# Kernel optimization log

Hardware: AMD Instinct MI355X
Metric: run time of the kernel (lower is better)

The kernel has to match this reference:

```python
import jax, jax.numpy as jnp
import numpy as np

N_NODES = 50000
N_EDGES = 800000
NF = 64       # input_nf = output_nf = hidden_nf
RADIAL = 1

def tanhshrink(x):
    return x - jnp.tanh(x)

def _linear_params(key, fan_in, fan_out):
    k1, k2 = jax.random.split(key)
    s = 1.0 / np.sqrt(fan_in)
    W = jax.random.uniform(k1, (fan_in, fan_out), jnp.float32, -s, s)
    b = jax.random.uniform(k2, (fan_out,), jnp.float32, -s, s)
    return W, b

def setup_inputs() -> dict:
    key = jax.random.key(0)
    ks = jax.random.split(key, 11)
    nodes = jax.random.normal(ks[0], (N_NODES, NF), jnp.float32)
    coord = jax.random.normal(ks[1], (N_NODES, 3), jnp.float32)
    edges = jax.random.randint(ks[2], (2, N_EDGES), 0, N_NODES, jnp.int64)
    # Edge MLP: Linear(2*NF + RADIAL -> NF), Linear(NF -> NF)
    eW1, eb1 = _linear_params(ks[3], 2 * NF + RADIAL, NF)
    eW2, eb2 = _linear_params(ks[4], NF, NF)
    # Edge attention: Linear(2*NF -> NF), Linear(NF -> 1)
    aW1, ab1 = _linear_params(ks[5], 2 * NF, NF)
    aW2, ab2 = _linear_params(ks[6], NF, 1)
    # Node MLP: Linear(NF + NF -> NF), Linear(NF -> NF)
    nW1, nb1 = _linear_params(ks[7], 2 * NF, NF)
    nW2, nb2 = _linear_params(ks[8], NF, NF)
    # Coord MLP: Linear(NF -> NF), Linear(NF -> 1)
    cW1, cb1 = _linear_params(ks[9], NF, NF)
    cW2, cb2 = _linear_params(ks[10], NF, 1)
    return dict(nodes=nodes, coord=coord, edges=edges,
                eW1=eW1, eb1=eb1, eW2=eW2, eb2=eb2,
                aW1=aW1, ab1=ab1, aW2=aW2, ab2=ab2,
                nW1=nW1, nb1=nb1, nW2=nW2, nb2=nb2,
                cW1=cW1, cb1=cb1, cW2=cW2, cb2=cb2)

def reference(nodes, coord, edges,
              eW1, eb1, eW2, eb2,
              aW1, ab1, aW2, ab2,
              nW1, nb1, nW2, nb2,
              cW1, cb1, cW2, cb2):
    row, col = edges[0], edges[1]
    n = nodes.shape[0]
    # Radial: squared distance along each edge
    rij = coord[row] - coord[col]                       # [E, 3]
    radial = jnp.sum(rij * rij, axis=1, keepdims=True)  # [E, 1]
    src, tgt = nodes[row], nodes[col]                   # [E, NF]
    # Edge MLP with attention gate
    agg_in = jnp.concatenate([src, tgt, radial], axis=1)
    h = tanhshrink(agg_in @ eW1 + eb1)
    h = tanhshrink(h @ eW2 + eb2)                       # [E, NF]
    att_in = jnp.concatenate([src, tgt], axis=1)
    a = tanhshrink(att_in @ aW1 + ab1)
    a = jax.nn.sigmoid(a @ aW2 + ab2)                   # [E, 1]
    edge_feat = h * a                                   # [E, NF]
    # Coordinate update: rij scaled by scalar per edge, scatter-add to row
    c = tanhshrink(edge_feat @ cW1 + cb1)
    trans = rij * (c @ cW2 + cb2)                       # [E, 3]
    coord_out = coord + jax.ops.segment_sum(trans, row, num_segments=n)
    # Node update: scatter-add edge features to row, residual MLP
    agg = jax.ops.segment_sum(edge_feat, row, num_segments=n)  # [N, NF]
    m = jnp.concatenate([nodes, agg], axis=1)
    m = tanhshrink(m @ nW1 + nb1)
    nodes_out = nodes + (m @ nW2 + nb2)
    return nodes_out, coord_out
```

## Files before the change

### kernel.cpp

```cpp
#include <hip/hip_runtime.h>
#include <hip/hip_fp16.h>

#define NF 64

typedef _Float16 half8 __attribute__((ext_vector_type(8)));
typedef float f32x4 __attribute__((ext_vector_type(4)));

__device__ __forceinline__ float ts_f(float x){
  float t = __expf(2.0f*x);
  float th = 1.0f - 2.0f*__builtin_amdgcn_rcpf(t + 1.0f);
  return x - th;
}
__device__ __forceinline__ float sigmoid_f(float x){
  return __builtin_amdgcn_rcpf(1.0f + __expf(-x));
}

__global__ __launch_bounds__(256) void k_prepw_hist(
    const float* __restrict__ eW1, const float* __restrict__ aW1,
    const float* __restrict__ eW2, const float* __restrict__ cW1,
    const float* __restrict__ nW1, const float* __restrict__ nW2,
    _Float16* __restrict__ W256t, _Float16* __restrict__ N1t,
    _Float16* __restrict__ W2t, _Float16* __restrict__ C1t,
    _Float16* __restrict__ N2t,
    const int* __restrict__ edges, int* __restrict__ counts,
    int* __restrict__ rank, int E,
    float4* __restrict__ zagg, int naggf4,
    float4* __restrict__ zcoord, int ncoordf4,
    int histB)
{
  const int bi = blockIdx.x;
  if (bi < 64){
    const int t = bi*256 + threadIdx.x;
    {
      const int n = t >> 6, k = t & 63;
      float v;
      if      (n < 64)  v = eW1[k*NF + n];
      else if (n < 128) v = aW1[k*NF + (n-64)];
      else if (n < 192) v = eW1[(64+k)*NF + (n-128)];
      else              v = aW1[(64+k)*NF + (n-192)];
      W256t[t] = (_Float16)v;
    }
    if (t < 64*128){
      const int n = t >> 7, k = t & 127;
      N1t[t] = (_Float16)nW1[k*NF + n];
    }
    if (t < 64*64){
      const int n = t >> 6, k = t & 63;
      W2t[t] = (_Float16)eW2[k*NF + n];
      C1t[t] = (_Float16)cW1[k*NF + n];
      N2t[t] = (_Float16)nW2[k*NF + n];
    }
  } else if (bi < 64 + histB){
    const int e = (bi - 64)*256 + threadIdx.x;
    if (e < E) rank[e] = atomicAdd(&counts[edges[e]], 1);
  } else {
    const float4 z = make_float4(0.f,0.f,0.f,0.f);
    const int nthr = (gridDim.x - 64 - histB) * 256;
    const int tid = (bi - 64 - histB)*256 + threadIdx.x;
    for (int i = tid; i < naggf4; i += nthr)   zagg[i] = z;
    for (int i = tid; i < ncoordf4; i += nthr) zcoord[i] = z;
  }
}

__global__ __launch_bounds__(256) void k_scan_zero(
    const int* __restrict__ counts, int* __restrict__ offs,
    int* __restrict__ btot, int* __restrict__ btop, int* __restrict__ done,
    const int* __restrict__ sentinel,
    int SCAN_B)
{
  const int t = threadIdx.x;
  const int b = blockIdx.x;

  __shared__ int s[256];
  __shared__ int isLast;
  const int BASE = *sentinel;
  const int4 c = *(const int4*)(counts + b*1024 + 4*t);
  const int c0 = c.x - BASE, c1 = c.y - BASE, c2 = c.z - BASE, c3 = c.w - BASE;
  const int mysum = c0 + c1 + c2 + c3;
  s[t] = mysum; __syncthreads();
  #pragma unroll
  for (int d=1; d<256; d<<=1){
    const int v = (t>=d) ? s[t-d] : 0; __syncthreads();
    s[t] += v; __syncthreads();
  }
  const int base = (t==0) ? 0 : s[t-1];
  int4 o;
  o.x = base; o.y = base + c0; o.z = o.y + c1; o.w = o.z + c2;
  *(int4*)(offs + b*1024 + 4*t) = o;
  if (t == 255) btot[b] = s[255];

  __threadfence();
  if (t == 0) isLast = (atomicAdd(done, 1) == BASE + SCAN_B - 1);
  __syncthreads();
  if (isLast){
    __threadfence();
    const int v = (t < SCAN_B) ? btot[t] : 0;
    s[t] = v; __syncthreads();
    #pragma unroll
    for (int d=1; d<256; d<<=1){
      const int u = (t>=d) ? s[t-d] : 0; __syncthreads();
      s[t] += u; __syncthreads();
    }
    if (t < SCAN_B) btop[t] = (t==0) ? 0 : s[t-1];
  }
}

__global__ __launch_bounds__(64, 8) void k_pre_scatter(
    const float* __restrict__ nodes,
    const float* __restrict__ eb1, const float* __restrict__ ab1,
    const _Float16* __restrict__ W256t,
    _Float16* __restrict__ P, _Float16* __restrict__ Q, int N,
    const int* __restrict__ edges, const int* __restrict__ offs,
    const int* __restrict__ btop, const int* __restrict__ rank,
    const int* __restrict__ sentinel,
    int* __restrict__ rs, int* __restrict__ cs, int E,
    int preBlocks)
{
  const int bi = blockIdx.x;
  const int lane = threadIdx.x;
  if (bi >= preBlocks){
    const int BASE = *sentinel;
    const int e = (bi - preBlocks)*64 + lane;
    if (e < E){
      const int r = edges[e], c = edges[E + e];
      const int pos = btop[r >> 10] + offs[r] + (rank[e] - BASE);
      rs[pos] = r; cs[pos] = c;
    }
    return;
  }

  const int p = lane & 15, q = lane >> 4;
  const int m0 = bi * 16;
  const int row = m0 + p;

  const float* __restrict__ xr = nodes + (size_t)row * NF;
  half8 A[2];
  #pragma unroll
  for (int kt=0; kt<2; kt++){
    const float4 xa = *(const float4*)(xr + kt*32 + q*8);
    const float4 xb = *(const float4*)(xr + kt*32 + q*8 + 4);
    A[kt][0]=(_Float16)xa.x; A[kt][1]=(_Float16)xa.y; A[kt][2]=(_Float16)xa.z; A[kt][3]=(_Float16)xa.w;
    A[kt][4]=(_Float16)xb.x; A[kt][5]=(_Float16)xb.y; A[kt][6]=(_Float16)xb.z; A[kt][7]=(_Float16)xb.w;
  }

  #pragma unroll
  for (int ni=0; ni<16; ni++){
    float b = 0.f;
    if (ni < 4)       b = eb1[16*ni + p];
    else if (ni < 8)  b = ab1[16*(ni-4) + p];
    f32x4 acc = (f32x4){b,b,b,b};
    #pragma unroll
    for (int kt=0; kt<2; kt++){
      const half8 Bf = *(const half8*)(W256t + (size_t)(16*ni + p)*NF + kt*32 + q*8);
      acc = __builtin_amdgcn_mfma_f32_16x16x32_f16(A[kt], Bf, acc, 0,0,0);
    }
    _Float16* __restrict__ dst = (ni < 8 ? P : Q);
    const int colbase = (ni & 7) * 16 + p;
    #pragma unroll
    for (int rr=0; rr<4; rr++)
      dst[(size_t)(m0 + 4*q + rr)*128 + colbase] = (_Float16)acc[rr];
  }
}

__global__ __launch_bounds__(64, 4) void egcl_edge(
    const float* __restrict__ coord,
    const int*   __restrict__ rs, const int* __restrict__ cs,
    const _Float16* __restrict__ P, const _Float16* __restrict__ Q,
    const float* __restrict__ eW1,
    const _Float16* __restrict__ W2t, const float* __restrict__ eb2,
    const float* __restrict__ aW2, const float* __restrict__ ab2,
    const _Float16* __restrict__ C1t, const float* __restrict__ cb1,
    const float* __restrict__ cW2, const float* __restrict__ cb2,
    _Float16* __restrict__ aggh, float* __restrict__ coord_out,
    int E)
{
  __shared__ _Float16 tile[64][72];
  __shared__ float gcbuf[64];

  const int lane = threadIdx.x;
  const int p = lane & 15, q = lane >> 4;
  const int e = blockIdx.x * 64 + lane;
  const bool valid = (e < E);
  const int el = valid ? e : (E - 1);

  const int r = rs[el];
  const int c = cs[el];
  const int rv = valid ? r : -1;

  const float rx = coord[3*r+0] - coord[3*c+0];
  const float ry = coord[3*r+1] - coord[3*c+1];
  const float rz = coord[3*r+2] - coord[3*c+2];
  const float radial = rx*rx + ry*ry + rz*rz;

  const _Float16* __restrict__ Pr = P + (size_t)r * 128;
  const _Float16* __restrict__ Qc = Q + (size_t)c * 128;
  const float* __restrict__ wrad = eW1 + 128*NF;

  half8 Bf[4][2];
  #pragma unroll
  for (int ni=0;ni<4;ni++)
    #pragma unroll
    for (int kt=0;kt<2;kt++)
      Bf[ni][kt] = *(const half8*)(W2t + (size_t)(16*ni + p)*NF + kt*32 + q*8);

  float sp0=0.f, sp1=0.f;
  #pragma unroll
  for (int g=0;g<8;g++){
    const half8 pa = *(const half8*)(Pr + 64 + 8*g);
    const half8 qa = *(const half8*)(Qc + 64 + 8*g);
    #pragma unroll
    for (int j=0;j<8;j++){
      const float v = ts_f((float)pa[j] + (float)qa[j]);
      if (j & 1) sp1 = fmaf(v, aW2[8*g+j], sp1); else sp0 = fmaf(v, aW2[8*g+j], sp0);
    }
  }
  const float gate = sigmoid_f(sp0 + sp1 + ab2[0]);
  gcbuf[lane] = gate;

  #pragma unroll
  for (int g=0;g<8;g++){
    const half8 ph = *(const half8*)(Pr + 8*g);
    const half8 qh = *(const half8*)(Qc + 8*g);
    half8 hv;
    #pragma unroll
    for (int j=0;j<8;j++)
      hv[j] = (_Float16)ts_f(fmaf(radial, wrad[8*g+j], (float)ph[j] + (float)qh[j]));
    *(half8*)&tile[lane][8*g] = hv;
  }
  __syncthreads();

  f32x4 acc[4][4];
  #pragma unroll
  for (int ni=0;ni<4;ni++){
    const float b = eb2[16*ni + p];
    #pragma unroll
    for (int mi=0;mi<4;mi++) acc[mi][ni] = (f32x4){b,b,b,b};
  }
  #pragma unroll
  for (int mi=0;mi<4;mi++){
    #pragma unroll
    for (int kt=0;kt<2;kt++){
      const half8 Af = *(const half8*)&tile[16*mi + p][kt*32 + q*8];
      #pragma unroll
      for (int ni=0;ni<4;ni++)
        acc[mi][ni] = __builtin_amdgcn_mfma_f32_16x16x32_f16(Af, Bf[ni][kt], acc[mi][ni], 0,0,0);
    }
  }
  __syncthreads();

  #pragma unroll
  for (int mi=0;mi<4;mi++){
    #pragma unroll
    for (int rr=0;rr<4;rr++){
      const int row = 16*mi + 4*q + rr;
      const float gv = gcbuf[row];
      #pragma unroll
      for (int ni=0;ni<4;ni++)
        tile[row][16*ni + p] = (_Float16)(ts_f(acc[mi][ni][rr]) * gv);
    }
  }

  #pragma unroll
  for (int ni=0;ni<4;ni++)
    #pragma unroll
    for (int kt=0;kt<2;kt++)
      Bf[ni][kt] = *(const half8*)(C1t + (size_t)(16*ni + p)*NF + kt*32 + q*8);
  #pragma unroll
  for (int ni=0;ni<4;ni++){
    const float b = cb1[16*ni + p];
    #pragma unroll
    for (int mi=0;mi<4;mi++) acc[mi][ni] = (f32x4){b,b,b,b};
  }
  __syncthreads();
  #pragma unroll
  for (int mi=0;mi<4;mi++){
    #pragma unroll
    for (int kt=0;kt<2;kt++){
      const half8 Af = *(const half8*)&tile[16*mi + p][kt*32 + q*8];
      #pragma unroll
      for (int ni=0;ni<4;ni++)
        acc[mi][ni] = __builtin_amdgcn_mfma_f32_16x16x32_f16(Af, Bf[ni][kt], acc[mi][ni], 0,0,0);
    }
  }

  float part[4][4];
  {
    float w2c[4];
    #pragma unroll
    for (int ni=0;ni<4;ni++) w2c[ni] = cW2[16*ni + p];
    #pragma unroll
    for (int mi=0;mi<4;mi++)
      #pragma unroll
      for (int rr=0;rr<4;rr++){
        float s = 0.f;
        #pragma unroll
        for (int ni=0;ni<4;ni++) s = fmaf(ts_f(acc[mi][ni][rr]), w2c[ni], s);
        part[mi][rr] = s;
      }
  }
  #pragma unroll
  for (int mask=1; mask<16; mask<<=1)
    #pragma unroll
    for (int mi=0;mi<4;mi++)
      #pragma unroll
      for (int rr=0;rr<4;rr++)
        part[mi][rr] += __shfl_xor(part[mi][rr], mask);
  {
    float v = 0.f;
    #pragma unroll
    for (int mi=0;mi<4;mi++)
      #pragma unroll
      for (int rr=0;rr<4;rr++)
        if (((p>>2)==mi) & ((p&3)==rr)) v = part[mi][rr];
    gcbuf[16*(p>>2) + 4*q + (p&3)] = v + cb2[0];
  }
  __syncthreads();

  const float cse = gcbuf[lane];

  unsigned long long bmask;
  {
    const int rvp = __shfl_up(rv, 1);
    const int fl = (lane == 0) || (rv != rvp);
    bmask = __ballot(fl);
  }

  {
    float tx = rx * cse, ty = ry * cse, tz = rz * cse;
    const int s = 63 - __builtin_clzll(bmask & ((2ull << lane) - 1ull));
    #pragma unroll
    for (int d=1; d<64; d<<=1){
      const float ux = __shfl_up(tx, d);
      const float uy = __shfl_up(ty, d);
      const float uz = __shfl_up(tz, d);
      if (lane >= d && (lane - d) >= s){ tx += ux; ty += uy; tz += uz; }
    }
    const int tail = (lane == 63) || (((bmask >> ((lane + 1) & 63)) & 1ull) && lane < 63);
    if (tail && rv >= 0){
      atomicAdd(coord_out + 3*rv + 0, tx);
      atomicAdd(coord_out + 3*rv + 1, ty);
      atomicAdd(coord_out + 3*rv + 2, tz);
    }
  }

  {
    int cur_r = __shfl(rv, 0);
    float runsum = 0.f;
    #pragma unroll
    for (int g8=0; g8<8; ++g8){
      _Float16 v[8];
      #pragma unroll
      for (int i=0;i<8;i++) v[i] = tile[g8*8 + i][lane];
      #pragma unroll
      for (int i=0;i<8;i++){
        const int eo = g8*8 + i;
        if (eo > 0 && ((bmask >> eo) & 1ull)){
          const float v0 = __shfl(runsum, 2*lane);
          const float v1 = __shfl(runsum, 2*lane+1);
          if (cur_r >= 0 && lane < 32){
            __half2 hv; hv.x = __float2half(v0); hv.y = __float2half(v1);
            unsafeAtomicAdd((__half2*)aggh + (size_t)cur_r*32 + lane, hv);
          }
          runsum = 0.f;
          cur_r = __shfl(rv, eo);
        }
        runsum += (float)v[i];
      }
    }
    const float v0 = __shfl(runsum, 2*lane);
    const float v1 = __shfl(runsum, 2*lane+1);
    if (cur_r >= 0 && lane < 32){
      __half2 hv; hv.x = __float2half(v0); hv.y = __float2half(v1);
      unsafeAtomicAdd((__half2*)aggh + (size_t)cur_r*32 + lane, hv);
    }
  }
}

__global__ __launch_bounds__(64, 8) void egcl_node(
    const float* __restrict__ nodes, const float* __restrict__ coord,
    const _Float16* __restrict__ aggh,
    const _Float16* __restrict__ N1t, const float* __restrict__ nb1,
    const _Float16* __restrict__ N2t, const float* __restrict__ nb2,
    float* __restrict__ out_nodes, float* __restrict__ out_coord, int N)
{
  __shared__ _Float16 t2[16][72];
  const int lane = threadIdx.x;
  const int p = lane & 15, q = lane >> 4;
  const int m0 = blockIdx.x * 16;
  const int row = m0 + p;

  half8 A[4];
  const float* __restrict__ xr = nodes + (size_t)row * NF;
  #pragma unroll
  for (int kt=0; kt<2; kt++){
    const float4 xa = *(const float4*)(xr + kt*32 + q*8);
    const float4 xb = *(const float4*)(xr + kt*32 + q*8 + 4);
    A[kt][0]=(_Float16)xa.x; A[kt][1]=(_Float16)xa.y; A[kt][2]=(_Float16)xa.z; A[kt][3]=(_Float16)xa.w;
    A[kt][4]=(_Float16)xb.x; A[kt][5]=(_Float16)xb.y; A[kt][6]=(_Float16)xb.z; A[kt][7]=(_Float16)xb.w;
  }
  const _Float16* __restrict__ ar = aggh + (size_t)row * NF;
  #pragma unroll
  for (int kt=2; kt<4; kt++)
    A[kt] = *(const half8*)(ar + (kt-2)*32 + q*8);

  f32x4 acc[4];
  #pragma unroll
  for (int ni=0;ni<4;ni++){
    const float b = nb1[16*ni + p];
    acc[ni] = (f32x4){b,b,b,b};
  }
  #pragma unroll
  for (int kt=0; kt<4; kt++){
    #pragma unroll
    for (int ni=0;ni<4;ni++){
      const half8 Bf = *(const half8*)(N1t + (size_t)(16*ni + p)*128 + kt*32 + q*8);
      acc[ni] = __builtin_amdgcn_mfma_f32_16x16x32_f16(A[kt], Bf, acc[ni], 0,0,0);
    }
  }

  #pragma unroll
  for (int ni=0;ni<4;ni++)
    #pragma unroll
    for (int rr=0;rr<4;rr++)
      t2[4*q + rr][16*ni + p] = (_Float16)ts_f(acc[ni][rr]);
  __syncthreads();

  half8 A2[2];
  #pragma unroll
  for (int kt=0; kt<2; kt++)
    A2[kt] = *(const half8*)&t2[p][kt*32 + q*8];

  f32x4 acc2[4];
  #pragma unroll
  for (int ni=0;ni<4;ni++){
    const float b = nb2[16*ni + p];
    acc2[ni] = (f32x4){b,b,b,b};
  }
  #pragma unroll
  for (int kt=0; kt<2; kt++){
    #pragma unroll
    for (int ni=0;ni<4;ni++){
      const half8 Bf = *(const half8*)(N2t + (size_t)(16*ni + p)*NF + kt*32 + q*8);
      acc2[ni] = __builtin_amdgcn_mfma_f32_16x16x32_f16(A2[kt], Bf, acc2[ni], 0,0,0);
    }
  }

  #pragma unroll
  for (int ni=0;ni<4;ni++){
    #pragma unroll
    for (int rr=0;rr<4;rr++){
      const size_t idx = (size_t)(m0 + 4*q + rr)*NF + 16*ni + p;
      out_nodes[idx] = nodes[idx] + acc2[ni][rr];
    }
  }

  if (lane < 48)
    out_coord[(size_t)m0*3 + lane] += coord[(size_t)m0*3 + lane];
}

extern "C" void kernel_launch(void* const* d_in, const int* in_sizes, int n_in,
                              void* d_out, int out_size, void* d_ws, size_t ws_size,
                              hipStream_t stream)
{
  const float* nodes = (const float*)d_in[0];
  const float* coord = (const float*)d_in[1];
  const int*   edges = (const int*)  d_in[2];
  const float* eW1 = (const float*)d_in[3];
  const float* eb1 = (const float*)d_in[4];
  const float* eW2 = (const float*)d_in[5];
  const float* eb2 = (const float*)d_in[6];
  const float* aW1 = (const float*)d_in[7];
  const float* ab1 = (const float*)d_in[8];
  const float* aW2 = (const float*)d_in[9];
  const float* ab2 = (const float*)d_in[10];
  const float* nW1 = (const float*)d_in[11];
  const float* nb1 = (const float*)d_in[12];
  const float* nW2 = (const float*)d_in[13];
  const float* nb2 = (const float*)d_in[14];
  const float* cW1 = (const float*)d_in[15];
  const float* cb1 = (const float*)d_in[16];
  const float* cW2 = (const float*)d_in[17];
  const float* cb2 = (const float*)d_in[18];

  const int E = in_sizes[2] / 2;
  const int N = in_sizes[0] / NF;
  const int SCAN_B = (N + 1023) >> 10;
  const int NBINS  = SCAN_B << 10;
  float* out_nodes = (float*)d_out;
  float* out_coord = out_nodes + (size_t)N * NF;

  char* w = (char*)d_ws;
  _Float16* P     = (_Float16*)w;  w += (size_t)N * 128 * 2;
  _Float16* Qh    = (_Float16*)w;  w += (size_t)N * 128 * 2;
  _Float16* aggh  = (_Float16*)w;  w += (size_t)N * 64 * 2;
  int* counts     = (int*)w;       w += (size_t)NBINS * 4;
  int* done       = (int*)w;       w += 64;
  int* sentinel   = (int*)w;       w += 64;
  int* offs       = (int*)w;       w += (size_t)NBINS * 4;
  int* btot       = (int*)w;       w += 256*4;
  int* btop       = (int*)w;       w += 256*4;
  int* rank       = (int*)w;       w += (size_t)E * 4;
  int* rs         = (int*)w;       w += (size_t)E * 4;
  int* cs_        = (int*)w;       w += (size_t)E * 4;
  _Float16* W256t = (_Float16*)w;  w += 256*64*2;
  _Float16* N1t   = (_Float16*)w;  w += 64*128*2;
  _Float16* W2t   = (_Float16*)w;  w += 64*64*2;
  _Float16* C1t   = (_Float16*)w;  w += 64*64*2;
  _Float16* N2t   = (_Float16*)w;  w += 64*64*2;

  const int histB = (E + 255)/256;
  const int naggf4   = (int)((size_t)N * 64 * 2 / 16);
  const int ncoordf4 = (N * 3) / 4;
  k_prepw_hist<<<64 + histB + 256, 256, 0, stream>>>(eW1, aW1, eW2, cW1, nW1, nW2,
      W256t, N1t, W2t, C1t, N2t, edges, counts, rank, E,
      (float4*)aggh, naggf4, (float4*)out_coord, ncoordf4, histB);

  k_scan_zero<<<SCAN_B, 256, 0, stream>>>(counts, offs, btot, btop, done,
      sentinel, SCAN_B);

  const int preBlocks = (N + 15)/16;
  const int scatBlocks = (E + 63)/64;
  k_pre_scatter<<<preBlocks + scatBlocks, 64, 0, stream>>>(nodes, eb1, ab1, W256t,
      P, Qh, N, edges, offs, btop, rank, sentinel, rs, cs_, E, preBlocks);

  egcl_edge<<<(E + 63)/64, 64, 0, stream>>>(coord, rs, cs_, P, Qh,
      eW1, W2t, eb2, aW2, ab2, C1t, cb1, cW2, cb2,
      aggh, out_coord, E);

  egcl_node<<<(N + 15)/16, 64, 0, stream>>>(nodes, coord, aggh,
      N1t, nb1, N2t, nb2, out_nodes, out_coord, N);
}
```

Measured before the change: 293.7 us.

## Use atomic offset claiming in scatter and pack row/col into int2

The histogram no longer records a per-edge rank array. The scatter step now claims positions with an atomicAdd on the per-node offsets, and writes row and column as a single int2 so the edge kernel does one 8-byte load instead of two separate ones. The per-edge gate is broadcast with a wavefront shuffle instead of a shared-memory buffer. This drops the rank array's write and read traffic and the sentinel read, in exchange for atomics in the scatter pass and a non-deterministic edge order within each row segment.

```diff
diff --git a/kernel.cpp b/kernel.cpp
--- a/kernel.cpp
+++ b/kernel.cpp
@@ -22,8 +22,7 @@
     _Float16* __restrict__ W256t, _Float16* __restrict__ N1t,
     _Float16* __restrict__ W2t, _Float16* __restrict__ C1t,
     _Float16* __restrict__ N2t,
-    const int* __restrict__ edges, int* __restrict__ counts,
-    int* __restrict__ rank, int E,
+    const int* __restrict__ edges, int* __restrict__ counts, int E,
     float4* __restrict__ zagg, int naggf4,
     float4* __restrict__ zcoord, int ncoordf4,
     int histB)
@@ -52,7 +51,7 @@
     }
   } else if (bi < 64 + histB){
     const int e = (bi - 64)*256 + threadIdx.x;
-    if (e < E) rank[e] = atomicAdd(&counts[edges[e]], 1);
+    if (e < E) atomicAdd(&counts[edges[e]], 1);
   } else {
     const float4 z = make_float4(0.f,0.f,0.f,0.f);
     const int nthr = (gridDim.x - 64 - histB) * 256;
@@ -110,21 +109,19 @@
     const float* __restrict__ eb1, const float* __restrict__ ab1,
     const _Float16* __restrict__ W256t,
     _Float16* __restrict__ P, _Float16* __restrict__ Q, int N,
-    const int* __restrict__ edges, const int* __restrict__ offs,
-    const int* __restrict__ btop, const int* __restrict__ rank,
-    const int* __restrict__ sentinel,
-    int* __restrict__ rs, int* __restrict__ cs, int E,
+    const int* __restrict__ edges, int* __restrict__ offs,
+    const int* __restrict__ btop,
+    int2* __restrict__ rc, int E,
     int preBlocks)
 {
   const int bi = blockIdx.x;
   const int lane = threadIdx.x;
   if (bi >= preBlocks){
-    const int BASE = *sentinel;
     const int e = (bi - preBlocks)*64 + lane;
     if (e < E){
       const int r = edges[e], c = edges[E + e];
-      const int pos = btop[r >> 10] + offs[r] + (rank[e] - BASE);
-      rs[pos] = r; cs[pos] = c;
+      const int pos = btop[r >> 10] + atomicAdd(&offs[r], 1);
+      rc[pos] = make_int2(r, c);
     }
     return;
   }
@@ -164,7 +161,7 @@
 
 __global__ __launch_bounds__(64, 4) void egcl_edge(
     const float* __restrict__ coord,
-    const int*   __restrict__ rs, const int* __restrict__ cs,
+    const int2*  __restrict__ rc,
     const _Float16* __restrict__ P, const _Float16* __restrict__ Q,
     const float* __restrict__ eW1,
     const _Float16* __restrict__ W2t, const float* __restrict__ eb2,
@@ -183,8 +180,9 @@
   const bool valid = (e < E);
   const int el = valid ? e : (E - 1);
 
-  const int r = rs[el];
-  const int c = cs[el];
+  const int2 rcv = rc[el];
+  const int r = rcv.x;
+  const int c = rcv.y;
   const int rv = valid ? r : -1;
 
   const float rx = coord[3*r+0] - coord[3*c+0];
@@ -215,7 +213,6 @@
     }
   }
   const float gate = sigmoid_f(sp0 + sp1 + ab2[0]);
-  gcbuf[lane] = gate;
 
   #pragma unroll
   for (int g=0;g<8;g++){
@@ -253,7 +250,7 @@
     #pragma unroll
     for (int rr=0;rr<4;rr++){
       const int row = 16*mi + 4*q + rr;
-      const float gv = gcbuf[row];
+      const float gv = __shfl(gate, row);
       #pragma unroll
       for (int ni=0;ni<4;ni++)
         tile[row][16*ni + p] = (_Float16)(ts_f(acc[mi][ni][rr]) * gv);
@@ -499,9 +496,7 @@
   int* offs       = (int*)w;       w += (size_t)NBINS * 4;
   int* btot       = (int*)w;       w += 256*4;
   int* btop       = (int*)w;       w += 256*4;
-  int* rank       = (int*)w;       w += (size_t)E * 4;
-  int* rs         = (int*)w;       w += (size_t)E * 4;
-  int* cs_        = (int*)w;       w += (size_t)E * 4;
+  int2* rc        = (int2*)w;      w += (size_t)E * 8;
   _Float16* W256t = (_Float16*)w;  w += 256*64*2;
   _Float16* N1t   = (_Float16*)w;  w += 64*128*2;
   _Float16* W2t   = (_Float16*)w;  w += 64*64*2;
@@ -512,7 +507,7 @@
   const int naggf4   = (int)((size_t)N * 64 * 2 / 16);
   const int ncoordf4 = (N * 3) / 4;
   k_prepw_hist<<<64 + histB + 256, 256, 0, stream>>>(eW1, aW1, eW2, cW1, nW1, nW2,
-      W256t, N1t, W2t, C1t, N2t, edges, counts, rank, E,
+      W256t, N1t, W2t, C1t, N2t, edges, counts, E,
       (float4*)aggh, naggf4, (float4*)out_coord, ncoordf4, histB);
 
   k_scan_zero<<<SCAN_B, 256, 0, stream>>>(counts, offs, btot, btop, done,
@@ -521,9 +516,9 @@
   const int preBlocks = (N + 15)/16;
   const int scatBlocks = (E + 63)/64;
   k_pre_scatter<<<preBlocks + scatBlocks, 64, 0, stream>>>(nodes, eb1, ab1, W256t,
-      P, Qh, N, edges, offs, btop, rank, sentinel, rs, cs_, E, preBlocks);
-
-  egcl_edge<<<(E + 63)/64, 64, 0, stream>>>(coord, rs, cs_, P, Qh,
+      P, Qh, N, edges, offs, btop, rc, E, preBlocks);
+
+  egcl_edge<<<(E + 63)/64, 64, 0, stream>>>(coord, rc, P, Qh,
       eW1, W2t, eb2, aW2, ab2, C1t, cb1, cW2, cb2,
       aggh, out_coord, E);
 
```

New measurement: 348.3 us. 1.19x slower.
